# Kernel optimization log

Hardware: AMD Instinct MI355X
Metric: run time of the kernel (lower is better)

## Reference

```python
import jax, jax.numpy as jnp
import numpy as np

EPS = 1e-5
NEG = -9e15

def layer_norm(x, gamma, beta):
    mu = jnp.mean(x, axis=-1, keepdims=True)
    var = jnp.var(x, axis=-1, keepdims=True)
    return (x - mu) * jax.lax.rsqrt(var + EPS) * gamma + beta

def setup_inputs() -> dict:
    key = jax.random.key(0)
    ks = jax.random.split(key, 8)
    B, S, D, F = 4, 4096, 128, 512
    q = jax.random.normal(ks[0], (B, S, D), dtype=jnp.float32)
    k = jax.random.normal(ks[1], (B, S, D), dtype=jnp.float32)
    v = jax.random.normal(ks[2], (B, S, D), dtype=jnp.float32)
    w1 = jax.random.normal(ks[3], (D, F), dtype=jnp.float32) / np.sqrt(D)
    b1 = jnp.zeros((F,), dtype=jnp.float32)
    w2 = jax.random.normal(ks[4], (F, D), dtype=jnp.float32) / np.sqrt(F)
    b2 = jnp.zeros((D,), dtype=jnp.float32)
    g1 = jnp.ones((D,), dtype=jnp.float32)
    be1 = jnp.zeros((D,), dtype=jnp.float32)
    g2 = jnp.ones((D,), dtype=jnp.float32)
    be2 = jnp.zeros((D,), dtype=jnp.float32)
    return {"q": q, "k": k, "v": v, "w1": w1, "b1": b1, "w2": w2, "b2": b2,
            "g1": g1, "be1": be1, "g2": g2, "be2": be2}

def reference(q, k, v, w1, b1, w2, b2, g1, be1, g2, be2):
    d_k = q.shape[-1]
    # naive attention: [B,S,S] logits materialized, as in the original
    logits = jnp.einsum('bqd,bkd->bqk', q, k) / jnp.sqrt(jnp.asarray(d_k, q.dtype))
    attn = jax.nn.softmax(logits, axis=-1)
    attn_out = jnp.einsum('bqk,bkd->bqd', attn, v)
    x = layer_norm(attn_out, g1, be1)
    ffn = jnp.maximum(x @ w1 + b1, 0) @ w2 + b2
    return layer_norm(x + ffn, g2, be2)
```

## Files before the change

### kernel.cpp

```cpp
#include <hip/hip_runtime.h>
#include <hip/hip_bf16.h>

typedef __attribute__((ext_vector_type(8))) __bf16 bf16x8;
typedef __attribute__((ext_vector_type(4))) __bf16 bf16x4;
typedef __attribute__((ext_vector_type(4))) float f32x4;
typedef __attribute__((ext_vector_type(16))) float f32x16;

#define MFMA16(a, b, c) __builtin_amdgcn_mfma_f32_16x16x32_bf16((a), (b), (c), 0, 0, 0)
#define MFMA32(a, b, c) __builtin_amdgcn_mfma_f32_32x32x16_bf16((a), (b), (c), 0, 0, 0)

static constexpr int S_LEN = 4096;
static constexpr int DH = 128;
static constexpr int NR = 4 * S_LEN;
static constexpr float QSCALE = 0.12752551286084110f;

__device__ inline bf16x8 pack8(float4 a, float4 b) {
  bf16x8 r;
  r[0] = (__bf16)a.x; r[1] = (__bf16)a.y; r[2] = (__bf16)a.z; r[3] = (__bf16)a.w;
  r[4] = (__bf16)b.x; r[5] = (__bf16)b.y; r[6] = (__bf16)b.z; r[7] = (__bf16)b.w;
  return r;
}

__device__ __forceinline__ float fexp2(float x) {
#if __has_builtin(__builtin_amdgcn_exp2f)
  return __builtin_amdgcn_exp2f(x);
#else
  return exp2f(x);
#endif
}

typedef __attribute__((address_space(1))) const unsigned GU32;
typedef __attribute__((address_space(3))) unsigned LU32;
__device__ __forceinline__ void gl16(const void* g, void* s) {
  __builtin_amdgcn_global_load_lds((GU32*)g, (LU32*)s, 16, 0, 0);
}

__global__ __launch_bounds__(256) void prep_all(
    const float* __restrict__ K, const float* __restrict__ V,
    const float* __restrict__ w1, const float* __restrict__ w2,
    __bf16* __restrict__ Kb, __bf16* __restrict__ VTb,
    __bf16* __restrict__ w1t, __bf16* __restrict__ w2t) {
  __shared__ float tile[32][33];
  const int bid = blockIdx.x;
  const int t = threadIdx.x;
  if (bid < 1024) {
    size_t i = ((size_t)bid * 256 + t) * 8;
    float4 a = *(const float4*)(K + i), b = *(const float4*)(K + i + 4);
    *(bf16x8*)(Kb + i) = pack8(a, b);
  } else if (bid < 3072) {
    const int bid2 = bid - 1024;
    const int b = bid2 >> 9, rem = bid2 & 511;
    const int s0 = (rem >> 2) * 32, d0 = (rem & 3) * 32;
    {
      int r = t >> 3, q = t & 7;
      float4 f = *(const float4*)(V + ((size_t)(b * S_LEN + s0 + r)) * DH + d0 + q * 4);
      tile[r][q * 4 + 0] = f.x; tile[r][q * 4 + 1] = f.y;
      tile[r][q * 4 + 2] = f.z; tile[r][q * 4 + 3] = f.w;
    }
    __syncthreads();
    {
      int dr = t >> 3, c2 = t & 7;
      bf16x4 u;
#pragma unroll
      for (int j = 0; j < 4; ++j) u[j] = (__bf16)tile[c2 * 4 + j][dr];
      *(bf16x4*)(VTb + ((size_t)(b * DH + d0 + dr)) * S_LEN + s0 + c2 * 4) = u;
    }
  } else {
    int i = (bid - 3072) * 256 + t;
    {
      int n = i >> 7, kk = i & 127;
      w1t[i] = (__bf16)w1[kk * 512 + n];
    }
    {
      int n = i >> 9, kk = i & 511;
      w2t[i] = (__bf16)w2[kk * 128 + n];
    }
  }
}

template <int NSP>
__global__ __launch_bounds__(256, 3) void attn_fa(
    const float* __restrict__ Q, const __bf16* __restrict__ Kb,
    const __bf16* __restrict__ VTb, __bf16* __restrict__ Op,
    float* __restrict__ lbuf) {
  constexpr int NTT = (S_LEN / NSP) / 64;
  __shared__ __attribute__((aligned(16))) __bf16 kl[2][64 * 128];
  __shared__ __attribute__((aligned(16))) __bf16 vt[2][128 * 64];
  __shared__ __attribute__((aligned(16))) __bf16 plds[4][32 * 64];

  const int tid = threadIdx.x;
  const int w = tid >> 6, l = tid & 63;
  const int q5 = l & 31, hi = l >> 5;
  const int bid = blockIdx.x;
  const int split = bid % NSP;
  const int qt = (bid / NSP) % 32;
  const int b = bid / (NSP * 32);
  const int R = b * S_LEN + qt * 128 + w * 32 + q5;
  const int kv0 = split * (S_LEN / NSP);

  bf16x8 qf[8];
  {
    const float* qp = Q + (size_t)R * DH + hi * 8;
#pragma unroll
    for (int kc = 0; kc < 8; ++kc) {
      float4 f0 = *(const float4*)(qp + kc * 16);
      float4 f1 = *(const float4*)(qp + kc * 16 + 4);
      f0.x *= QSCALE; f0.y *= QSCALE; f0.z *= QSCALE; f0.w *= QSCALE;
      f1.x *= QSCALE; f1.y *= QSCALE; f1.z *= QSCALE; f1.w *= QSCALE;
      qf[kc] = pack8(f0, f1);
    }
  }

  f32x16 o[4];
#pragma unroll
  for (int db = 0; db < 4; ++db) o[db] = f32x16{};
  float lsum = 0.f;

  const __bf16* kbase = Kb + (size_t)b * S_LEN * DH;
  const __bf16* vbase = VTb + (size_t)b * DH * S_LEN;

#define STAGE(BUF, S_OFF)                                                      \
  {                                                                            \
    _Pragma("unroll") for (int i = 0; i < 4; ++i) {                            \
      int r = w * 16 + i * 4 + (l >> 4);                                       \
      gl16(kbase + (size_t)((S_OFF) + r) * DH + (((l & 15) * 8) ^ ((r & 7) << 3)), \
           &kl[BUF][(w * 16 + i * 4) * 128]);                                  \
    }                                                                          \
    _Pragma("unroll") for (int i = 0; i < 4; ++i) {                            \
      int d = w * 32 + i * 8 + (l >> 3);                                       \
      gl16(vbase + (size_t)d * S_LEN + (S_OFF) + (((l & 7) * 8) ^ ((d & 7) << 3)), \
           &vt[BUF][(w * 32 + i * 8) * 64]);                                   \
    }                                                                          \
  }

  STAGE(0, kv0);
  __syncthreads();

  const int pswz = (q5 & 7) << 3;
  __bf16* pl = &plds[w][0];

  int cur = 0;
  for (int t = 0; t < NTT; ++t) {
    if (t + 1 < NTT) STAGE(cur ^ 1, kv0 + (t + 1) * 64);

#pragma unroll
    for (int kvb = 0; kvb < 2; ++kvb) {
      f32x16 acc = f32x16{};
      const int row = kvb * 32 + q5;
#pragma unroll
      for (int kc = 0; kc < 8; ++kc) {
        bf16x8 kf = *(const bf16x8*)&kl[cur][(row * 128 + kc * 16 + hi * 8) ^ pswz];
        acc = MFMA32(kf, qf[kc], acc);
      }
#pragma unroll
      for (int t4 = 0; t4 < 4; ++t4) {
        bf16x4 pk;
#pragma unroll
        for (int qi = 0; qi < 4; ++qi) {
          float e = fexp2(acc[4 * t4 + qi]);
          lsum += e;
          pk[qi] = (__bf16)e;
        }
        *(bf16x4*)&pl[(q5 * 64 + kvb * 32 + t4 * 8 + hi * 4) ^ pswz] = pk;
      }
    }

    bf16x8 pb[4];
#pragma unroll
    for (int kc = 0; kc < 4; ++kc)
      pb[kc] = *(const bf16x8*)&pl[(q5 * 64 + kc * 16 + hi * 8) ^ pswz];
#pragma unroll
    for (int db = 0; db < 4; ++db) {
      const int row = db * 32 + q5;
#pragma unroll
      for (int kc = 0; kc < 4; ++kc) {
        bf16x8 vf = *(const bf16x8*)&vt[cur][(row * 64 + kc * 16 + hi * 8) ^ pswz];
        o[db] = MFMA32(vf, pb[kc], o[db]);
      }
    }

    __syncthreads();
    cur ^= 1;
  }
#undef STAGE

  lsum += __shfl_xor(lsum, 32);
  const float inv = 1.f / lsum;
  __bf16* orow = Op + ((size_t)split * NR + R) * DH;
#pragma unroll
  for (int db = 0; db < 4; ++db)
#pragma unroll
    for (int t4 = 0; t4 < 4; ++t4) {
      bf16x4 pk;
#pragma unroll
      for (int qi = 0; qi < 4; ++qi) pk[qi] = (__bf16)(o[db][4 * t4 + qi] * inv);
      *(bf16x4*)(orow + db * 32 + t4 * 8 + hi * 4) = pk;
    }
  if (hi == 0) lbuf[(size_t)split * NR + R] = lsum;
}

__global__ __launch_bounds__(256) void ffn_fused(
    const __bf16* __restrict__ Op, const float* __restrict__ lbuf,
    const float* __restrict__ g1, const float* __restrict__ be1,
    const __bf16* __restrict__ w1t, const __bf16* __restrict__ w2t,
    const float* __restrict__ b1, const float* __restrict__ b2,
    const float* __restrict__ g2, const float* __restrict__ be2,
    float* __restrict__ Out, int nsp) {
  __shared__ __attribute__((aligned(16))) __bf16 xl[16 * 128];
  __shared__ float xr[16][132];
  __shared__ __attribute__((aligned(16))) __bf16 hl[16 * 512];
  __shared__ float part[4][16][2];

  const int tid = threadIdx.x;
  const int w = tid >> 6, l = tid & 63, lg = l >> 4, lc = l & 15;
  const int row0 = blockIdx.x * 16;

  {
    const int prow = tid >> 4, pc8 = tid & 15;
    const int R = row0 + prow;
    float v[8] = {0.f, 0.f, 0.f, 0.f, 0.f, 0.f, 0.f, 0.f};
    float den = 0.f;
    for (int s = 0; s < nsp; ++s) {
      float ls = lbuf[(size_t)s * NR + R];
      den += ls;
      bf16x8 p = *(const bf16x8*)(Op + ((size_t)s * NR + R) * DH + pc8 * 8);
#pragma unroll
      for (int j = 0; j < 8; ++j) v[j] += ls * (float)p[j];
    }
    float inv = 1.f / den;
    float sm = 0.f, sq = 0.f;
#pragma unroll
    for (int j = 0; j < 8; ++j) {
      v[j] *= inv;
      sm += v[j];
      sq += v[j] * v[j];
    }
#pragma unroll
    for (int d = 1; d < 16; d <<= 1) {
      sm += __shfl_xor(sm, d);
      sq += __shfl_xor(sq, d);
    }
    float mu = sm * (1.f / 128.f);
    float var = sq * (1.f / 128.f) - mu * mu;
    float rs = rsqrtf(var + 1e-5f);
    float4 ga = *(const float4*)(g1 + pc8 * 8), gb = *(const float4*)(g1 + pc8 * 8 + 4);
    float4 ba = *(const float4*)(be1 + pc8 * 8), bb = *(const float4*)(be1 + pc8 * 8 + 4);
    float gv[8] = {ga.x, ga.y, ga.z, ga.w, gb.x, gb.y, gb.z, gb.w};
    float bv[8] = {ba.x, ba.y, ba.z, ba.w, bb.x, bb.y, bb.z, bb.w};
    bf16x8 xb;
    float xo[8];
#pragma unroll
    for (int j = 0; j < 8; ++j) {
      xo[j] = (v[j] - mu) * rs * gv[j] + bv[j];
      xb[j] = (__bf16)xo[j];
    }
    *(bf16x8*)&xl[(prow * 128 + pc8 * 8) ^ ((prow & 7) << 3)] = xb;
    *(float4*)&xr[prow][pc8 * 8] = make_float4(xo[0], xo[1], xo[2], xo[3]);
    *(float4*)&xr[prow][pc8 * 8 + 4] = make_float4(xo[4], xo[5], xo[6], xo[7]);
  }
  __syncthreads();

  bf16x8 xf[4];
  const int m = lc;
#pragma unroll
  for (int kc = 0; kc < 4; ++kc)
    xf[kc] = *(const bf16x8*)&xl[(m * 128 + kc * 32 + lg * 8) ^ ((m & 7) << 3)];

#pragma unroll
  for (int nb = 0; nb < 8; ++nb) {
    int n0 = w * 128 + nb * 16 + lc;
    const __bf16* wp = w1t + (size_t)n0 * 128 + lg * 8;
    f32x4 acc = (f32x4){0.f, 0.f, 0.f, 0.f};
#pragma unroll
    for (int kc = 0; kc < 4; ++kc)
      acc = MFMA16(xf[kc], *(const bf16x8*)(wp + kc * 32), acc);
    float bias = b1[n0];
#pragma unroll
    for (int r = 0; r < 4; ++r) {
      int rr = lg * 4 + r;
      hl[rr * 512 + (n0 ^ (lg << 4))] = (__bf16)fmaxf(acc[r] + bias, 0.f);
    }
  }
  __syncthreads();

  const int col0 = w * 32 + lc;
  f32x4 oo[2];
#pragma unroll
  for (int nb2 = 0; nb2 < 2; ++nb2) {
    int d0 = col0 + nb2 * 16;
    const __bf16* wp2 = w2t + (size_t)d0 * 512 + lg * 8;
    f32x4 acc = (f32x4){0.f, 0.f, 0.f, 0.f};
#pragma unroll
    for (int kc = 0; kc < 16; ++kc) {
      bf16x8 ha = *(const bf16x8*)&hl[lc * 512 + ((kc * 32 + lg * 8) ^ ((lc >> 2) << 4))];
      acc = MFMA16(ha, *(const bf16x8*)(wp2 + kc * 32), acc);
    }
    oo[nb2] = acc;
  }

  float b2v[2] = {b2[col0], b2[col0 + 16]};
  float g2v[2] = {g2[col0], g2[col0 + 16]};
  float be2v[2] = {be2[col0], be2[col0 + 16]};
  float sum[4] = {0.f, 0.f, 0.f, 0.f}, sq[4] = {0.f, 0.f, 0.f, 0.f};
#pragma unroll
  for (int nb2 = 0; nb2 < 2; ++nb2)
#pragma unroll
    for (int r = 0; r < 4; ++r) {
      int rr = lg * 4 + r;
      float xv = xr[rr][col0 + nb2 * 16];
      float tv = oo[nb2][r] + b2v[nb2] + xv;
      oo[nb2][r] = tv;
      sum[r] += tv;
      sq[r] += tv * tv;
    }
#pragma unroll
  for (int r = 0; r < 4; ++r) {
#pragma unroll
    for (int d = 1; d < 16; d <<= 1) {
      sum[r] += __shfl_xor(sum[r], d);
      sq[r] += __shfl_xor(sq[r], d);
    }
    if (lc == 0) {
      part[w][lg * 4 + r][0] = sum[r];
      part[w][lg * 4 + r][1] = sq[r];
    }
  }
  __syncthreads();

#pragma unroll
  for (int r = 0; r < 4; ++r) {
    int rr = lg * 4 + r;
    float S = 0.f, Qq = 0.f;
#pragma unroll
    for (int ww = 0; ww < 4; ++ww) {
      S += part[ww][rr][0];
      Qq += part[ww][rr][1];
    }
    float mu = S * (1.f / 128.f);
    float var = Qq * (1.f / 128.f) - mu * mu;
    float rs = rsqrtf(var + 1e-5f);
#pragma unroll
    for (int nb2 = 0; nb2 < 2; ++nb2)
      Out[(size_t)(row0 + rr) * DH + col0 + nb2 * 16] =
          (oo[nb2][r] - mu) * rs * g2v[nb2] + be2v[nb2];
  }
}

extern "C" void kernel_launch(void* const* d_in, const int* in_sizes, int n_in,
                              void* d_out, int out_size, void* d_ws, size_t ws_size,
                              hipStream_t stream) {
  const float* Q = (const float*)d_in[0];
  const float* K = (const float*)d_in[1];
  const float* V = (const float*)d_in[2];
  const float* w1 = (const float*)d_in[3];
  const float* b1 = (const float*)d_in[4];
  const float* w2 = (const float*)d_in[5];
  const float* b2 = (const float*)d_in[6];
  const float* g1 = (const float*)d_in[7];
  const float* be1 = (const float*)d_in[8];
  const float* g2 = (const float*)d_in[9];
  const float* be2 = (const float*)d_in[10];
  float* Out = (float*)d_out;

  char* p = (char*)d_ws;
  __bf16* w1t = (__bf16*)p;  p += 512 * 128 * 2;
  __bf16* w2t = (__bf16*)p;  p += 128 * 512 * 2;
  __bf16* Kb  = (__bf16*)p;  p += (size_t)NR * DH * 2;
  __bf16* VTb = (__bf16*)p;  p += (size_t)NR * DH * 2;
  float* lbuf = (float*)p;   p += (size_t)8 * NR * 4;
  __bf16* Op  = (__bf16*)p;

  const size_t base = (size_t)(p - (char*)d_ws);
  const size_t need8 = base + (size_t)8 * NR * DH * 2;
  const int nsp = (ws_size >= need8) ? 8 : 4;

  prep_all<<<3328, 256, 0, stream>>>(K, V, w1, w2, Kb, VTb, w1t, w2t);
  if (nsp == 8)
    attn_fa<8><<<4 * 32 * 8, 256, 0, stream>>>(Q, Kb, VTb, Op, lbuf);
  else
    attn_fa<4><<<4 * 32 * 4, 256, 0, stream>>>(Q, Kb, VTb, Op, lbuf);
  ffn_fused<<<NR / 16, 256, 0, stream>>>(Op, lbuf, g1, be1, w1t, w2t, b1, b2,
                                         g2, be2, Out, nsp);
}
```

Baseline: 104.1 us.

## Halve attention KV tile to 32 rows to raise occupancy, template split count in FFN

Shrinks the per-iteration KV tile in the flash-attention kernel from 64 to 32 keys. This halves the K/V/P shared-memory buffers and raises the launch-bounds occupancy target from 3 to 4 blocks per CU. The V-transpose staging and the P tile swizzle are reworked to fit the new 32-wide layout. The FFN kernel now takes the split count as a template parameter so its reduction loop fully unrolls. The cost is twice as many loop iterations and barriers per block, with less MFMA work between syncs, and tighter register limits that could cause spills.

New measurement: 146.5 us. +40.8%, slower.

```diff
diff --git a/kernel.cpp b/kernel.cpp
--- a/kernel.cpp
+++ b/kernel.cpp
@@ -79,14 +79,14 @@
 }
 
 template <int NSP>
-__global__ __launch_bounds__(256, 3) void attn_fa(
+__global__ __launch_bounds__(256, 4) void attn_fa(
     const float* __restrict__ Q, const __bf16* __restrict__ Kb,
     const __bf16* __restrict__ VTb, __bf16* __restrict__ Op,
     float* __restrict__ lbuf) {
-  constexpr int NTT = (S_LEN / NSP) / 64;
-  __shared__ __attribute__((aligned(16))) __bf16 kl[2][64 * 128];
-  __shared__ __attribute__((aligned(16))) __bf16 vt[2][128 * 64];
-  __shared__ __attribute__((aligned(16))) __bf16 plds[4][32 * 64];
+  constexpr int NTT = (S_LEN / NSP) / 32;
+  __shared__ __attribute__((aligned(16))) __bf16 kl[2][32 * 128];
+  __shared__ __attribute__((aligned(16))) __bf16 vt[2][64 * 64];
+  __shared__ __attribute__((aligned(16))) __bf16 plds[4][32 * 32];
 
   const int tid = threadIdx.x;
   const int w = tid >> 6, l = tid & 63;
@@ -121,60 +121,60 @@
 
 #define STAGE(BUF, S_OFF)                                                      \
   {                                                                            \
-    _Pragma("unroll") for (int i = 0; i < 4; ++i) {                            \
-      int r = w * 16 + i * 4 + (l >> 4);                                       \
+    _Pragma("unroll") for (int i = 0; i < 2; ++i) {                            \
+      int r = w * 8 + i * 4 + (l >> 4);                                        \
       gl16(kbase + (size_t)((S_OFF) + r) * DH + (((l & 15) * 8) ^ ((r & 7) << 3)), \
-           &kl[BUF][(w * 16 + i * 4) * 128]);                                  \
+           &kl[BUF][(w * 8 + i * 4) * 128]);                                   \
     }                                                                          \
-    _Pragma("unroll") for (int i = 0; i < 4; ++i) {                            \
-      int d = w * 32 + i * 8 + (l >> 3);                                       \
-      gl16(vbase + (size_t)d * S_LEN + (S_OFF) + (((l & 7) * 8) ^ ((d & 7) << 3)), \
-           &vt[BUF][(w * 32 + i * 8) * 64]);                                   \
+    _Pragma("unroll") for (int i = 0; i < 2; ++i) {                            \
+      int rr = w * 16 + i * 8 + (l >> 3);                                      \
+      int cp = (l & 7) ^ (rr & 7);                                             \
+      int d = (cp >> 2) * 64 + rr;                                             \
+      gl16(vbase + (size_t)d * S_LEN + (S_OFF) + (cp & 3) * 8,                 \
+           &vt[BUF][(w * 16 + i * 8) * 64]);                                   \
     }                                                                          \
   }
 
   STAGE(0, kv0);
   __syncthreads();
 
-  const int pswz = (q5 & 7) << 3;
+  const int swz = (q5 & 7) << 3;
   __bf16* pl = &plds[w][0];
 
   int cur = 0;
   for (int t = 0; t < NTT; ++t) {
-    if (t + 1 < NTT) STAGE(cur ^ 1, kv0 + (t + 1) * 64);
-
-#pragma unroll
-    for (int kvb = 0; kvb < 2; ++kvb) {
-      f32x16 acc = f32x16{};
-      const int row = kvb * 32 + q5;
-#pragma unroll
-      for (int kc = 0; kc < 8; ++kc) {
-        bf16x8 kf = *(const bf16x8*)&kl[cur][(row * 128 + kc * 16 + hi * 8) ^ pswz];
-        acc = MFMA32(kf, qf[kc], acc);
+    if (t + 1 < NTT) STAGE(cur ^ 1, kv0 + (t + 1) * 32);
+
+    f32x16 acc = f32x16{};
+#pragma unroll
+    for (int kc = 0; kc < 8; ++kc) {
+      bf16x8 kf = *(const bf16x8*)&kl[cur][(q5 * 128 + kc * 16 + hi * 8) ^ swz];
+      acc = MFMA32(kf, qf[kc], acc);
+    }
+
+#pragma unroll
+    for (int t4 = 0; t4 < 4; ++t4) {
+      bf16x4 pk;
+#pragma unroll
+      for (int qi = 0; qi < 4; ++qi) {
+        float e = fexp2(acc[4 * t4 + qi]);
+        lsum += e;
+        pk[qi] = (__bf16)e;
       }
-#pragma unroll
-      for (int t4 = 0; t4 < 4; ++t4) {
-        bf16x4 pk;
-#pragma unroll
-        for (int qi = 0; qi < 4; ++qi) {
-          float e = fexp2(acc[4 * t4 + qi]);
-          lsum += e;
-          pk[qi] = (__bf16)e;
-        }
-        *(bf16x4*)&pl[(q5 * 64 + kvb * 32 + t4 * 8 + hi * 4) ^ pswz] = pk;
-      }
-    }
-
-    bf16x8 pb[4];
-#pragma unroll
-    for (int kc = 0; kc < 4; ++kc)
-      pb[kc] = *(const bf16x8*)&pl[(q5 * 64 + kc * 16 + hi * 8) ^ pswz];
+      *(bf16x4*)&pl[q5 * 32 + ((t4 ^ (q5 & 3)) << 3) + 4 * hi] = pk;
+    }
+
+    bf16x8 pb[2];
+#pragma unroll
+    for (int kc = 0; kc < 2; ++kc)
+      pb[kc] = *(const bf16x8*)&pl[q5 * 32 + (((2 * kc + hi) ^ (q5 & 3)) << 3)];
 #pragma unroll
     for (int db = 0; db < 4; ++db) {
-      const int row = db * 32 + q5;
-#pragma unroll
-      for (int kc = 0; kc < 4; ++kc) {
-        bf16x8 vf = *(const bf16x8*)&vt[cur][(row * 64 + kc * 16 + hi * 8) ^ pswz];
+      const int rr = (db & 1) * 32 + q5;
+      const int dhi = db >> 1;
+#pragma unroll
+      for (int kc = 0; kc < 2; ++kc) {
+        bf16x8 vf = *(const bf16x8*)&vt[cur][(rr * 64 + dhi * 32 + kc * 16 + hi * 8) ^ swz];
         o[db] = MFMA32(vf, pb[kc], o[db]);
       }
     }
@@ -199,13 +199,14 @@
   if (hi == 0) lbuf[(size_t)split * NR + R] = lsum;
 }
 
+template <int NSP>
 __global__ __launch_bounds__(256) void ffn_fused(
     const __bf16* __restrict__ Op, const float* __restrict__ lbuf,
     const float* __restrict__ g1, const float* __restrict__ be1,
     const __bf16* __restrict__ w1t, const __bf16* __restrict__ w2t,
     const float* __restrict__ b1, const float* __restrict__ b2,
     const float* __restrict__ g2, const float* __restrict__ be2,
-    float* __restrict__ Out, int nsp) {
+    float* __restrict__ Out) {
   __shared__ __attribute__((aligned(16))) __bf16 xl[16 * 128];
   __shared__ float xr[16][132];
   __shared__ __attribute__((aligned(16))) __bf16 hl[16 * 512];
@@ -220,7 +221,8 @@
     const int R = row0 + prow;
     float v[8] = {0.f, 0.f, 0.f, 0.f, 0.f, 0.f, 0.f, 0.f};
     float den = 0.f;
-    for (int s = 0; s < nsp; ++s) {
+#pragma unroll
+    for (int s = 0; s < NSP; ++s) {
       float ls = lbuf[(size_t)s * NR + R];
       den += ls;
       bf16x8 p = *(const bf16x8*)(Op + ((size_t)s * NR + R) * DH + pc8 * 8);
@@ -375,10 +377,13 @@
   const int nsp = (ws_size >= need8) ? 8 : 4;
 
   prep_all<<<3328, 256, 0, stream>>>(K, V, w1, w2, Kb, VTb, w1t, w2t);
-  if (nsp == 8)
+  if (nsp == 8) {
     attn_fa<8><<<4 * 32 * 8, 256, 0, stream>>>(Q, Kb, VTb, Op, lbuf);
-  else
+    ffn_fused<8><<<NR / 16, 256, 0, stream>>>(Op, lbuf, g1, be1, w1t, w2t, b1,
+                                              b2, g2, be2, Out);
+  } else {
     attn_fa<4><<<4 * 32 * 4, 256, 0, stream>>>(Q, Kb, VTb, Op, lbuf);
-  ffn_fused<<<NR / 16, 256, 0, stream>>>(Op, lbuf, g1, be1, w1t, w2t, b1, b2,
-                                         g2, be2, Out, nsp);
-}
+    ffn_fused<4><<<NR / 16, 256, 0, stream>>>(Op, lbuf, g1, be1, w1t, w2t, b1,
+                                              b2, g2, be2, Out);
+  }
+}
```

## Stage K/V tiles through registers into single LDS buffer instead of direct-to-LDS double buffer

Applied to the files above, without the earlier changes.

The attention kernel stops using global_load_lds into two LDS buffers. It now prefetches the next K/V tile into registers, then writes it into a single LDS buffer after a barrier, which adds a second __syncthreads per iteration. This cuts LDS use, which may allow more blocks per CU, at the cost of extra VGPRs and one more barrier. The FFN kernel is also templated on the split count so the merge loop over splits can be fully unrolled.

Result: slower. 205.3 us (+97.3%).

```diff
diff --git a/kernel.cpp b/kernel.cpp
--- a/kernel.cpp
+++ b/kernel.cpp
@@ -27,12 +27,6 @@
 #else
   return exp2f(x);
 #endif
-}
-
-typedef __attribute__((address_space(1))) const unsigned GU32;
-typedef __attribute__((address_space(3))) unsigned LU32;
-__device__ __forceinline__ void gl16(const void* g, void* s) {
-  __builtin_amdgcn_global_load_lds((GU32*)g, (LU32*)s, 16, 0, 0);
 }
 
 __global__ __launch_bounds__(256) void prep_all(
@@ -84,8 +78,8 @@
     const __bf16* __restrict__ VTb, __bf16* __restrict__ Op,
     float* __restrict__ lbuf) {
   constexpr int NTT = (S_LEN / NSP) / 64;
-  __shared__ __attribute__((aligned(16))) __bf16 kl[2][64 * 128];
-  __shared__ __attribute__((aligned(16))) __bf16 vt[2][128 * 64];
+  __shared__ __attribute__((aligned(16))) __bf16 kl[64 * 128];
+  __shared__ __attribute__((aligned(16))) __bf16 vt[128 * 64];
   __shared__ __attribute__((aligned(16))) __bf16 plds[4][32 * 64];
 
   const int tid = threadIdx.x;
@@ -119,29 +113,43 @@
   const __bf16* kbase = Kb + (size_t)b * S_LEN * DH;
   const __bf16* vbase = VTb + (size_t)b * DH * S_LEN;
 
-#define STAGE(BUF, S_OFF)                                                      \
+  bf16x8 kreg[4], vreg[4];
+
+#define LOAD_TILES(S_OFF)                                                      \
   {                                                                            \
     _Pragma("unroll") for (int i = 0; i < 4; ++i) {                            \
       int r = w * 16 + i * 4 + (l >> 4);                                       \
-      gl16(kbase + (size_t)((S_OFF) + r) * DH + (((l & 15) * 8) ^ ((r & 7) << 3)), \
-           &kl[BUF][(w * 16 + i * 4) * 128]);                                  \
+      kreg[i] = *(const bf16x8*)(kbase + (size_t)((S_OFF) + r) * DH +          \
+                                 (((l & 15) * 8) ^ ((r & 7) << 3)));           \
     }                                                                          \
     _Pragma("unroll") for (int i = 0; i < 4; ++i) {                            \
       int d = w * 32 + i * 8 + (l >> 3);                                       \
-      gl16(vbase + (size_t)d * S_LEN + (S_OFF) + (((l & 7) * 8) ^ ((d & 7) << 3)), \
-           &vt[BUF][(w * 32 + i * 8) * 64]);                                   \
+      vreg[i] = *(const bf16x8*)(vbase + (size_t)d * S_LEN + (S_OFF) +         \
+                                 (((l & 7) * 8) ^ ((d & 7) << 3)));            \
     }                                                                          \
   }
-
-  STAGE(0, kv0);
+#define WRITE_TILES()                                                          \
+  {                                                                            \
+    _Pragma("unroll") for (int i = 0; i < 4; ++i) {                            \
+      int r = w * 16 + i * 4 + (l >> 4);                                       \
+      *(bf16x8*)&kl[r * 128 + (l & 15) * 8] = kreg[i];                         \
+    }                                                                          \
+    _Pragma("unroll") for (int i = 0; i < 4; ++i) {                            \
+      int d = w * 32 + i * 8 + (l >> 3);                                       \
+      *(bf16x8*)&vt[d * 64 + (l & 7) * 8] = vreg[i];                           \
+    }                                                                          \
+  }
+
+  LOAD_TILES(kv0);
+  WRITE_TILES();
   __syncthreads();
 
-  const int pswz = (q5 & 7) << 3;
+  const int swz = (q5 & 7) << 3;
   __bf16* pl = &plds[w][0];
 
-  int cur = 0;
   for (int t = 0; t < NTT; ++t) {
-    if (t + 1 < NTT) STAGE(cur ^ 1, kv0 + (t + 1) * 64);
+    const bool more = (t + 1 < NTT);
+    if (more) LOAD_TILES(kv0 + (t + 1) * 64);
 
 #pragma unroll
     for (int kvb = 0; kvb < 2; ++kvb) {
@@ -149,7 +157,7 @@
       const int row = kvb * 32 + q5;
 #pragma unroll
       for (int kc = 0; kc < 8; ++kc) {
-        bf16x8 kf = *(const bf16x8*)&kl[cur][(row * 128 + kc * 16 + hi * 8) ^ pswz];
+        bf16x8 kf = *(const bf16x8*)&kl[(row * 128 + kc * 16 + hi * 8) ^ swz];
         acc = MFMA32(kf, qf[kc], acc);
       }
 #pragma unroll
@@ -161,28 +169,32 @@
           lsum += e;
           pk[qi] = (__bf16)e;
         }
-        *(bf16x4*)&pl[(q5 * 64 + kvb * 32 + t4 * 8 + hi * 4) ^ pswz] = pk;
+        *(bf16x4*)&pl[(q5 * 64 + kvb * 32 + t4 * 8 + hi * 4) ^ swz] = pk;
       }
     }
 
     bf16x8 pb[4];
 #pragma unroll
     for (int kc = 0; kc < 4; ++kc)
-      pb[kc] = *(const bf16x8*)&pl[(q5 * 64 + kc * 16 + hi * 8) ^ pswz];
+      pb[kc] = *(const bf16x8*)&pl[(q5 * 64 + kc * 16 + hi * 8) ^ swz];
 #pragma unroll
     for (int db = 0; db < 4; ++db) {
       const int row = db * 32 + q5;
 #pragma unroll
       for (int kc = 0; kc < 4; ++kc) {
-        bf16x8 vf = *(const bf16x8*)&vt[cur][(row * 64 + kc * 16 + hi * 8) ^ pswz];
+        bf16x8 vf = *(const bf16x8*)&vt[(row * 64 + kc * 16 + hi * 8) ^ swz];
         o[db] = MFMA32(vf, pb[kc], o[db]);
       }
     }
 
     __syncthreads();
-    cur ^= 1;
-  }
-#undef STAGE
+    if (more) {
+      WRITE_TILES();
+      __syncthreads();
+    }
+  }
+#undef LOAD_TILES
+#undef WRITE_TILES
 
   lsum += __shfl_xor(lsum, 32);
   const float inv = 1.f / lsum;
@@ -199,13 +211,14 @@
   if (hi == 0) lbuf[(size_t)split * NR + R] = lsum;
 }
 
+template <int NSP>
 __global__ __launch_bounds__(256) void ffn_fused(
     const __bf16* __restrict__ Op, const float* __restrict__ lbuf,
     const float* __restrict__ g1, const float* __restrict__ be1,
     const __bf16* __restrict__ w1t, const __bf16* __restrict__ w2t,
     const float* __restrict__ b1, const float* __restrict__ b2,
     const float* __restrict__ g2, const float* __restrict__ be2,
-    float* __restrict__ Out, int nsp) {
+    float* __restrict__ Out) {
   __shared__ __attribute__((aligned(16))) __bf16 xl[16 * 128];
   __shared__ float xr[16][132];
   __shared__ __attribute__((aligned(16))) __bf16 hl[16 * 512];
@@ -220,7 +233,8 @@
     const int R = row0 + prow;
     float v[8] = {0.f, 0.f, 0.f, 0.f, 0.f, 0.f, 0.f, 0.f};
     float den = 0.f;
-    for (int s = 0; s < nsp; ++s) {
+#pragma unroll
+    for (int s = 0; s < NSP; ++s) {
       float ls = lbuf[(size_t)s * NR + R];
       den += ls;
       bf16x8 p = *(const bf16x8*)(Op + ((size_t)s * NR + R) * DH + pc8 * 8);
@@ -375,10 +389,13 @@
   const int nsp = (ws_size >= need8) ? 8 : 4;
 
   prep_all<<<3328, 256, 0, stream>>>(K, V, w1, w2, Kb, VTb, w1t, w2t);
-  if (nsp == 8)
+  if (nsp == 8) {
     attn_fa<8><<<4 * 32 * 8, 256, 0, stream>>>(Q, Kb, VTb, Op, lbuf);
-  else
+    ffn_fused<8><<<NR / 16, 256, 0, stream>>>(Op, lbuf, g1, be1, w1t, w2t, b1,
+                                              b2, g2, be2, Out);
+  } else {
     attn_fa<4><<<4 * 32 * 4, 256, 0, stream>>>(Q, Kb, VTb, Op, lbuf);
-  ffn_fused<<<NR / 16, 256, 0, stream>>>(Op, lbuf, g1, be1, w1t, w2t, b1, b2,
-                                         g2, be2, Out, nsp);
-}
+    ffn_fused<4><<<NR / 16, 256, 0, stream>>>(Op, lbuf, g1, be1, w1t, w2t, b1,
+                                              b2, g2, be2, Out);
+  }
+}
```
